# Kernel tuning notes

Hardware: AMD Instinct MI355X
Metric: run time of the kernel (lower is better)

## Reference

```python
import jax, jax.numpy as jnp
import numpy as np
import math


def _conv2d(x, w, b):
    # 3x3, stride 1, pad 1, NCHW / OIHW
    y = jax.lax.conv_general_dilated(x, w, (1, 1), ((1, 1), (1, 1)),
                                     dimension_numbers=('NCHW', 'OIHW', 'NCHW'))
    return y + b[None, :, None, None]


def _avgpool2(x):
    B, C, H, W = x.shape
    return x.reshape(B, C, H // 2, 2, W // 2, 2).mean(axis=(3, 5))


def setup_inputs() -> dict:
    key = jax.random.key(0)
    ks = jax.random.split(key, 12)
    B, H, W = 8, 512, 512
    x = jax.random.uniform(ks[0], (B, 3, H, W), dtype=jnp.float32)

    def conv_w(k, o, i):
        return jax.random.normal(k, (o, i, 3, 3), jnp.float32) / jnp.sqrt(jnp.float32(i * 9))

    def lin_w(k, o, i):
        return jax.random.normal(k, (o, i), jnp.float32) / jnp.sqrt(jnp.float32(i))

    return {
        'x': x,
        'w1': conv_w(ks[1], 16, 6),  'b1': jnp.zeros((16,), jnp.float32),
        'w2': conv_w(ks[2], 32, 16), 'b2': jnp.zeros((32,), jnp.float32),
        'w3': conv_w(ks[3], 64, 32), 'b3': jnp.zeros((64,), jnp.float32),
        'fw1': lin_w(ks[4], 256, 64),  'fb1': jnp.zeros((256,), jnp.float32),
        'fw2': lin_w(ks[5], 100, 256), 'fb2': jnp.zeros((100,), jnp.float32),
    }


def reference(x, w1, b1, w2, b2, w3, b3, fw1, fb1, fw2, fb2):
    B, C, H, W = x.shape
    # radial distance from image center (torch.meshgrid default = 'ij')
    a, b = jnp.meshgrid(jnp.arange(H), jnp.arange(W), indexing='ij')
    dist = jnp.sqrt((a - H / 2) ** 2 + (b - W / 2) ** 2).astype(jnp.float32)
    max_radius = math.sqrt(H * H + W * W) / 2

    xf = jnp.fft.fftn(x, axes=(-1, -2))
    # torch.fft.fftshift with no dim shifts ALL axes (incl. B, C); jnp matches.
    xf = jnp.fft.fftshift(xf)
    x_mag = jnp.log10(jnp.abs(xf) + 1)

    fi = jnp.concatenate([x, x_mag], axis=1)  # [B,6,H,W]
    y = jax.nn.relu(_conv2d(fi, w1, b1))
    y = _avgpool2(y)
    y = jax.nn.relu(_conv2d(y, w2, b2))
    y = _avgpool2(y)
    y = _conv2d(y, w3, b3)
    y = y.mean(axis=(2, 3))  # AdaptiveAvgPool2d((1,1)) -> [B,64]
    # note: NO activation between the two FC layers in the original
    value_set = jax.nn.leaky_relu((y @ fw1.T + fb1) @ fw2.T + fb2, 0.01)  # [B,100]

    # 100 radial ring bins; replace the 100-iter where-loop with bucketize+gather
    radius_set = max_radius * (jnp.arange(100, dtype=jnp.float32) + 1.0) * 0.01
    # bin i: radius_set[i-1] < dist <= radius_set[i]  ==  searchsorted left
    bin_idx = jnp.clip(jnp.searchsorted(radius_set, dist, side='left'), 0, 99)  # [H,W]
    fq_mask = value_set[:, bin_idx]  # [B,H,W] gather, same math as sum of ring masks

    low = xf * fq_mask[:, None, :, :]
    low = jnp.fft.ifftshift(low)
    low = jnp.fft.ifftn(low, axes=(-1, -2))
    lowpass = jnp.clip(low.real, 0.0, 1.0)
    return lowpass, fq_mask, value_set
```

## Files before the change

### kernel.cpp

```cpp
#include <hip/hip_runtime.h>
#include <math.h>

#define NPIX 262144
#define FSTR 513

__device__ __forceinline__ int brev9(int i) { return (int)(__brev((unsigned)i) >> 23); }

__device__ __forceinline__ void init_tw(float* twr, float* twi, int t) {
  if (t < 256) {
    float ang = -3.14159265358979323846f * (float)t / 256.0f;
    float s, c;
    sincosf(ang, &s, &c);
    twr[t] = c; twi[t] = s;
  }
}

template<bool FWD>
__device__ __forceinline__ void fft512x8(float* __restrict__ sr, float* __restrict__ si,
                                         const float* __restrict__ twr,
                                         const float* __restrict__ twi, int t) {
  const int c  = t >> 5;
  const int tq = t & 31;
  float* cr = sr + c * FSTR;
  float* ci = si + c * FSTR;
  #pragma unroll
  for (int sp = 0; sp < 4; sp++) {
    const int s = 2 * sp;
    const int h = 1 << s;
    __syncthreads();
    #pragma unroll
    for (int m = 0; m < 4; m++) {
      int q = tq + 32 * m;
      int j = q & (h - 1);
      int base = ((q >> s) << (s + 2)) | j;
      int i1 = j << (8 - s);
      int i2 = j << (7 - s);
      float w1r = twr[i1], w1i = FWD ? twi[i1] : -twi[i1];
      float w2r = twr[i2], w2i = FWD ? twi[i2] : -twi[i2];
      float ar = cr[base],         ai = ci[base];
      float br = cr[base + h],     bi = ci[base + h];
      float c2r = cr[base + 2*h],  c2i = ci[base + 2*h];
      float dr = cr[base + 3*h],   di = ci[base + 3*h];
      float wbr = br * w1r - bi * w1i, wbi = br * w1i + bi * w1r;
      float wdr = dr * w1r - di * w1i, wdi = dr * w1i + di * w1r;
      float t0r = ar + wbr,  t0i = ai + wbi;
      float t1r = ar - wbr,  t1i = ai - wbi;
      float t2r = c2r + wdr, t2i = c2i + wdi;
      float t3r = c2r - wdr, t3i = c2i - wdi;
      float u2r = t2r * w2r - t2i * w2i, u2i = t2r * w2i + t2i * w2r;
      float v3r = t3r * w2r - t3i * w2i, v3i = t3r * w2i + t3i * w2r;
      float u3r = FWD ? v3i : -v3i;
      float u3i = FWD ? -v3r : v3r;
      cr[base]         = t0r + u2r;  ci[base]         = t0i + u2i;
      cr[base + 2*h]   = t0r - u2r;  ci[base + 2*h]   = t0i - u2i;
      cr[base + h]     = t1r + u3r;  ci[base + h]     = t1i + u3i;
      cr[base + 3*h]   = t1r - u3r;  ci[base + 3*h]   = t1i - u3i;
    }
  }
  __syncthreads();
  #pragma unroll
  for (int m = 0; m < 8; m++) {
    int k = tq + 32 * m;
    float wr = twr[k], wi = FWD ? twi[k] : -twi[k];
    float vr = cr[k + 256], vi = ci[k + 256];
    float tr = vr * wr - vi * wi;
    float ti = vr * wi + vi * wr;
    float ur = cr[k], ui = ci[k];
    cr[k] = ur + tr;        ci[k] = ui + ti;
    cr[k + 256] = ur - tr;  ci[k + 256] = ui - ti;
  }
  __syncthreads();
}

__global__ __launch_bounds__(256) void k_fft_rows(const float* __restrict__ x,
                                                  float2* __restrict__ xf) {
  __shared__ float sr[8 * FSTR], si[8 * FSTR], twr[256], twi[256];
  int t = threadIdx.x;
  int img = blockIdx.x >> 6;
  int r0 = (blockIdx.x & 63) << 3;
  init_tw(twr, twi, t);
  const float4* p4 = (const float4*)(x + (size_t)img * NPIX + (size_t)r0 * 512);
  for (int e = t; e < 1024; e += 256) {
    int row = e >> 7, w = e & 127;
    float4 f = p4[e];
    float* cr = sr + row * FSTR;
    float* ci = si + row * FSTR;
    int p = 4 * w;
    cr[brev9(p)]     = f.x;  ci[brev9(p)]     = 0.0f;
    cr[brev9(p + 1)] = f.y;  ci[brev9(p + 1)] = 0.0f;
    cr[brev9(p + 2)] = f.z;  ci[brev9(p + 2)] = 0.0f;
    cr[brev9(p + 3)] = f.w;  ci[brev9(p + 3)] = 0.0f;
  }
  fft512x8<true>(sr, si, twr, twi, t);
  float4* q4 = (float4*)(xf + (size_t)img * NPIX + (size_t)r0 * 512);
  for (int e = t; e < 2048; e += 256) {
    int row = e >> 8, u = e & 255;
    const float* cr = sr + row * FSTR;
    const float* ci = si + row * FSTR;
    q4[e] = make_float4(cr[2 * u], ci[2 * u], cr[2 * u + 1], ci[2 * u + 1]);
  }
}

__global__ __launch_bounds__(256) void k_fft_cols(float2* __restrict__ xf,
                                                  float* __restrict__ xmag) {
  __shared__ float sr[8 * FSTR], si[8 * FSTR], twr[256], twi[256];
  int t = threadIdx.x;
  int img = blockIdx.x >> 6;
  int c0 = (blockIdx.x & 63) << 3;
  init_tw(twr, twi, t);
  float2* base = xf + (size_t)img * NPIX + c0;
  const int q = t & 3;
  const int j = (t >> 2) & 15;
  const int w = t >> 6;
  #pragma unroll
  for (int it = 0; it < 8; it++) {
    int row = 32 * j + 4 * it + w;
    float4 f = *(const float4*)(base + (size_t)row * 512 + 2 * q);
    int rr = brev9(row);
    sr[(2 * q) * FSTR + rr]     = f.x;  si[(2 * q) * FSTR + rr]     = f.y;
    sr[(2 * q + 1) * FSTR + rr] = f.z;  si[(2 * q + 1) * FSTR + rr] = f.w;
  }
  fft512x8<true>(sr, si, twr, twi, t);
  int sb = img / 3, sc = img - 3 * sb;
  int dimg = ((sb + 4) & 7) * 3 + (sc + 1) % 3;
  float* xb = xmag + (size_t)dimg * NPIX + (c0 ^ 256);
  const int rg = t >> 2;
  #pragma unroll
  for (int it = 0; it < 8; it++) {
    int row = 64 * it + rg;
    float a0 = sr[(2 * q) * FSTR + row],     b0 = si[(2 * q) * FSTR + row];
    float a1 = sr[(2 * q + 1) * FSTR + row], b1 = si[(2 * q + 1) * FSTR + row];
    *(float4*)(base + (size_t)row * 512 + 2 * q) = make_float4(a0, b0, a1, b1);
    float m0 = log10f(sqrtf(a0 * a0 + b0 * b0) + 1.0f);
    float m1 = log10f(sqrtf(a1 * a1 + b1 * b1) + 1.0f);
    *(float2*)(xb + (size_t)(row ^ 256) * 512 + 2 * q) = make_float2(m0, m1);
  }
}

__global__ __launch_bounds__(256) void k_conv1(const float* __restrict__ x,
                                               const float* __restrict__ xmag,
                                               const float* __restrict__ w1,
                                               const float* __restrict__ b1,
                                               float* __restrict__ out) {
  __shared__ float tile[2][18 * 132 + 8];
  const int t = threadIdx.x;
  const int tx = t & 31, ty = t >> 5;
  const int PC0 = blockIdx.x * 64;
  const int PR0 = blockIdx.y * 8;
  const int b  = blockIdx.z >> 1;
  const int og = (blockIdx.z & 1) * 8;
  const int R0 = PR0 * 2 - 1;
  const int C0 = PC0 * 2 - 1;

  int li[10], gi[10];
  bool okf[10];
  #pragma unroll
  for (int k = 0; k < 10; k++) {
    int e = t + 256 * k;
    bool valid = e < 2340;
    int i = e / 130, j = e - i * 130;
    int rr = R0 + i, cc = C0 + j;
    bool ok = valid && ((unsigned)rr < 512u) && ((unsigned)cc < 512u);
    li[k] = valid ? (i * 132 + j) : (18 * 132);
    gi[k] = ok ? (rr * 512 + cc) : 0;
    okf[k] = ok;
  }

  float acc[8][8];
  #pragma unroll
  for (int o = 0; o < 8; o++)
    #pragma unroll
    for (int q = 0; q < 8; q++) acc[o][q] = 0.0f;

  const float* xb = x + (size_t)(b * 3) * NPIX;
  const float* mb = xmag + (size_t)(b * 3) * NPIX;

  float ld[10];
  #pragma unroll
  for (int k = 0; k < 10; k++) ld[k] = okf[k] ? xb[gi[k]] : 0.0f;
  #pragma unroll
  for (int k = 0; k < 10; k++) tile[0][li[k]] = ld[k];
  __syncthreads();

  for (int ic = 0; ic < 6; ic++) {
    if (ic < 5) {
      const float* sn = (ic + 1 < 3) ? (xb + (size_t)(ic + 1) * NPIX)
                                     : (mb + (size_t)(ic - 2) * NPIX);
      #pragma unroll
      for (int k = 0; k < 10; k++) ld[k] = okf[k] ? sn[gi[k]] : 0.0f;
    }
    const float* cur = tile[ic & 1];
    float patch[4][6];
    #pragma unroll
    for (int dy = 0; dy < 4; dy++) {
      const float* rp = cur + (2 * ty + dy) * 132 + 4 * tx;
      float4 f = *(const float4*)rp;
      float2 g = *(const float2*)(rp + 4);
      patch[dy][0] = f.x; patch[dy][1] = f.y; patch[dy][2] = f.z;
      patch[dy][3] = f.w; patch[dy][4] = g.x; patch[dy][5] = g.y;
    }
    #pragma unroll
    for (int o = 0; o < 8; o++) {
      const float* wk = w1 + (size_t)((og + o) * 6 + ic) * 9;
      float k0 = wk[0], k1 = wk[1], k2 = wk[2], k3 = wk[3], k4 = wk[4],
            k5 = wk[5], k6 = wk[6], k7 = wk[7], k8 = wk[8];
      #pragma unroll
      for (int py = 0; py < 2; py++)
        #pragma unroll
        for (int px = 0; px < 4; px++) {
          acc[o][py * 4 + px] +=
              k0 * patch[py][px]     + k1 * patch[py][px + 1]     + k2 * patch[py][px + 2]
            + k3 * patch[py + 1][px] + k4 * patch[py + 1][px + 1] + k5 * patch[py + 1][px + 2]
            + k6 * patch[py + 2][px] + k7 * patch[py + 2][px + 1] + k8 * patch[py + 2][px + 2];
        }
    }
    if (ic < 5) {
      float* nxt = tile[(ic + 1) & 1];
      #pragma unroll
      for (int k = 0; k < 10; k++) nxt[li[k]] = ld[k];
      __syncthreads();
    }
  }
  #pragma unroll
  for (int o = 0; o < 8; o++) {
    float bias = b1[og + o];
    float p0 = fmaxf(acc[o][0] + bias, 0.0f) + fmaxf(acc[o][1] + bias, 0.0f)
             + fmaxf(acc[o][4] + bias, 0.0f) + fmaxf(acc[o][5] + bias, 0.0f);
    float p1 = fmaxf(acc[o][2] + bias, 0.0f) + fmaxf(acc[o][3] + bias, 0.0f)
             + fmaxf(acc[o][6] + bias, 0.0f) + fmaxf(acc[o][7] + bias, 0.0f);
    float2* q = (float2*)(out + ((size_t)(b * 16 + og + o) * 256 + PR0 + ty) * 256 + PC0 + 2 * tx);
    *q = make_float2(p0 * 0.25f, p1 * 0.25f);
  }
}

__global__ __launch_bounds__(256) void k_conv2(const float* __restrict__ in,
                                               const float* __restrict__ w2,
                                               const float* __restrict__ b2,
                                               float* __restrict__ S) {
  __shared__ float tile[2][18 * 68 + 8];
  __shared__ float wsum[4][8];
  const int t = threadIdx.x;
  const int tx = t & 31, ty = t >> 5;
  const int bx = blockIdx.x, by = blockIdx.y;
  const int PC0 = bx * 32;
  const int PR0 = by * 8;
  const int b  = blockIdx.z >> 2;
  const int og = (blockIdx.z & 3) * 8;
  const int R0 = PR0 * 2 - 1;
  const int C0 = PC0 * 2 - 1;

  int li[5], gi[5];
  bool okf[5];
  #pragma unroll
  for (int k = 0; k < 5; k++) {
    int e = t + 256 * k;
    bool valid = e < 1188;
    int i = e / 66, j = e - 66 * i;
    int rr = R0 + i, cc = C0 + j;
    bool ok = valid && ((unsigned)rr < 256u) && ((unsigned)cc < 256u);
    li[k] = valid ? (i * 68 + j) : (18 * 68);
    gi[k] = ok ? (rr * 256 + cc) : 0;
    okf[k] = ok;
  }

  float acc[8][4];
  #pragma unroll
  for (int o = 0; o < 8; o++)
    #pragma unroll
    for (int q = 0; q < 4; q++) acc[o][q] = 0.0f;

  const float* inb = in + (size_t)(b * 16) * 65536;

  float ld[5];
  #pragma unroll
  for (int k = 0; k < 5; k++) ld[k] = okf[k] ? inb[gi[k]] : 0.0f;
  #pragma unroll
  for (int k = 0; k < 5; k++) tile[0][li[k]] = ld[k];
  __syncthreads();

  for (int ic = 0; ic < 16; ic++) {
    if (ic < 15) {
      const float* sn = inb + (size_t)(ic + 1) * 65536;
      #pragma unroll
      for (int k = 0; k < 5; k++) ld[k] = okf[k] ? sn[gi[k]] : 0.0f;
    }
    const float* cur = tile[ic & 1];
    float patch[4][4];
    #pragma unroll
    for (int dy = 0; dy < 4; dy++) {
      const float* rp = cur + (2 * ty + dy) * 68 + 2 * tx;
      float2 f0 = *(const float2*)rp;
      float2 f1 = *(const float2*)(rp + 2);
      patch[dy][0] = f0.x; patch[dy][1] = f0.y;
      patch[dy][2] = f1.x; patch[dy][3] = f1.y;
    }
    #pragma unroll
    for (int o = 0; o < 8; o++) {
      const float* wk = w2 + (size_t)((og + o) * 16 + ic) * 9;
      float k0 = wk[0], k1 = wk[1], k2 = wk[2], k3 = wk[3], k4 = wk[4],
            k5 = wk[5], k6 = wk[6], k7 = wk[7], k8 = wk[8];
      #pragma unroll
      for (int py = 0; py < 2; py++)
        #pragma unroll
        for (int px = 0; px < 2; px++) {
          acc[o][py * 2 + px] +=
              k0 * patch[py][px]     + k1 * patch[py][px + 1]     + k2 * patch[py][px + 2]
            + k3 * patch[py + 1][px] + k4 * patch[py + 1][px + 1] + k5 * patch[py + 1][px + 2]
            + k6 * patch[py + 2][px] + k7 * patch[py + 2][px + 1] + k8 * patch[py + 2][px + 2];
        }
    }
    if (ic < 15) {
      float* nxt = tile[(ic + 1) & 1];
      #pragma unroll
      for (int k = 0; k < 5; k++) nxt[li[k]] = ld[k];
      __syncthreads();
    }
  }

  const int lane = t & 63;
  const int wid = t >> 6;
  float* Sb0 = S + (size_t)(b * 32 + og) * 9;
  #pragma unroll
  for (int o = 0; o < 8; o++) {
    float bias = b2[og + o];
    float v = (fmaxf(acc[o][0] + bias, 0.0f) + fmaxf(acc[o][1] + bias, 0.0f)
             + fmaxf(acc[o][2] + bias, 0.0f) + fmaxf(acc[o][3] + bias, 0.0f)) * 0.25f;
    float* Sb = Sb0 + o * 9;
    float ts = v;
    #pragma unroll
    for (int off = 32; off > 0; off >>= 1) ts += __shfl_down(ts, off);
    if (lane == 0) wsum[wid][o] = ts;
    if (by == 0) {
      float e = (ty == 0) ? v : 0.0f;
      #pragma unroll
      for (int off = 32; off > 0; off >>= 1) e += __shfl_down(e, off);
      if (lane == 0) atomicAdd(&Sb[1], e);
    }
    if (by == 15) {
      float e = (ty == 7) ? v : 0.0f;
      #pragma unroll
      for (int off = 32; off > 0; off >>= 1) e += __shfl_down(e, off);
      if (lane == 0) atomicAdd(&Sb[2], e);
    }
    if (bx == 0 && tx == 0)  atomicAdd(&Sb[3], v);
    if (bx == 3 && tx == 31) atomicAdd(&Sb[4], v);
    if (bx == 0 && by == 0  && t == 0)   Sb[5] = v;
    if (bx == 3 && by == 0  && t == 31)  Sb[6] = v;
    if (bx == 0 && by == 15 && t == 224) Sb[7] = v;
    if (bx == 3 && by == 15 && t == 255) Sb[8] = v;
  }
  __syncthreads();
  if (t < 8)
    atomicAdd(&Sb0[t * 9], wsum[0][t] + wsum[1][t] + wsum[2][t] + wsum[3][t]);
}

__global__ __launch_bounds__(256) void k_fc(const float* __restrict__ S,
                                            const float* __restrict__ w3,
                                            const float* __restrict__ b3,
                                            const float* __restrict__ fw1,
                                            const float* __restrict__ fb1,
                                            const float* __restrict__ fw2,
                                            const float* __restrict__ fb2,
                                            float* __restrict__ vs_out) {
  __shared__ float Sp[2304];
  __shared__ float y[512];
  __shared__ float h1[2048];
  int t = threadIdx.x;
  for (int e = t; e < 2304; e += 256) {
    int cell = e / 9, k = e - 9 * cell;
    int dy = k / 3, dx = k - 3 * dy;
    const float* s = S + cell * 9;
    float v = s[0];
    if (dy == 0) v -= s[2];
    if (dy == 2) v -= s[1];
    if (dx == 0) v -= s[4];
    if (dx == 2) v -= s[3];
    if (dy == 0 && dx == 0) v += s[8];
    if (dy == 0 && dx == 2) v += s[7];
    if (dy == 2 && dx == 0) v += s[6];
    if (dy == 2 && dx == 2) v += s[5];
    Sp[e] = v;
  }
  __syncthreads();
  for (int e = t; e < 512; e += 256) {
    int b = e >> 6, o = e & 63;
    const float* wrow = w3 + (size_t)o * 288;
    const float* sp = Sp + b * 288;
    float s = 0.0f;
    #pragma unroll 4
    for (int k = 0; k < 288; k++) s += wrow[k] * sp[k];
    y[e] = b3[o] + s * (1.0f / 16384.0f);
  }
  __syncthreads();
  for (int e = t; e < 2048; e += 256) {
    int b = e >> 8, j = e & 255;
    float s = fb1[j];
    for (int k = 0; k < 64; k++) s += y[b * 64 + k] * fw1[j * 64 + k];
    h1[e] = s;
  }
  __syncthreads();
  for (int e = t; e < 800; e += 256) {
    int b = e / 100, i = e - 100 * b;
    float s = fb2[i];
    for (int j = 0; j < 256; j++) s += h1[b * 256 + j] * fw2[i * 256 + j];
    vs_out[e] = (s >= 0.0f) ? s : 0.01f * s;
  }
}

__global__ __launch_bounds__(256) void k_mask(const float* __restrict__ vs,
                                              float* __restrict__ fq_mask) {
  int idx = blockIdx.x * 256 + threadIdx.x;
  int h = idx >> 9, w = idx & 511;
  float da = (float)h - 256.0f, db = (float)w - 256.0f;
  float dist = sqrtf(da * da + db * db);
  int lo = 0, hi = 100;
  while (lo < hi) {
    int mid = (lo + hi) >> 1;
    float r = (362.03867196751236f * (float)(mid + 1)) * 0.01f;
    if (r < dist) lo = mid + 1; else hi = mid;
  }
  int bin = lo > 99 ? 99 : lo;
  #pragma unroll
  for (int b = 0; b < 8; b++)
    fq_mask[(size_t)b * NPIX + idx] = vs[b * 100 + bin];
}

__global__ __launch_bounds__(256) void k_ifft_rows_mod(float2* __restrict__ xf,
                                                       const float* __restrict__ fq_mask) {
  __shared__ float sr[8 * FSTR], si[8 * FSTR], twr[256], twi[256];
  int t = threadIdx.x;
  int img = blockIdx.x >> 6;
  int r0 = (blockIdx.x & 63) << 3;
  int bm = ((img / 3) + 4) & 7;
  init_tw(twr, twi, t);
  const float* mbase = fq_mask + (size_t)bm * NPIX;
  float4* base4 = (float4*)(xf + (size_t)img * NPIX + (size_t)r0 * 512);
  for (int e = t; e < 2048; e += 256) {
    int u = (e & 3) | (((e >> 2) & 15) << 3) | (((e >> 6) & 1) << 2) | (((e >> 7) & 1) << 7);
    int row = e >> 8;
    float4 f = base4[row * 256 + u];
    int p0 = 2 * u;
    const float* mrow = mbase + (size_t)((r0 + row + 256) & 511) * 512;
    float2 m = *(const float2*)(mrow + ((p0 + 256) & 511));
    int rr0 = brev9(p0);
    float* cr = sr + row * FSTR;
    float* ci = si + row * FSTR;
    cr[rr0]       = f.x * m.x;  ci[rr0]       = f.y * m.x;
    cr[rr0 + 256] = f.z * m.y;  ci[rr0 + 256] = f.w * m.y;
  }
  fft512x8<false>(sr, si, twr, twi, t);
  for (int e = t; e < 2048; e += 256) {
    int row = e >> 8, u = e & 255;
    const float* cr = sr + row * FSTR;
    const float* ci = si + row * FSTR;
    base4[e] = make_float4(cr[2 * u], ci[2 * u], cr[2 * u + 1], ci[2 * u + 1]);
  }
}

__global__ __launch_bounds__(256) void k_ifft_cols_out(const float2* __restrict__ xf,
                                                       float* __restrict__ lowpass) {
  __shared__ float sr[8 * FSTR], si[8 * FSTR], twr[256], twi[256];
  int t = threadIdx.x;
  int img = blockIdx.x >> 6;
  int c0 = (blockIdx.x & 63) << 3;
  init_tw(twr, twi, t);
  const float2* base = xf + (size_t)img * NPIX + c0;
  const int q = t & 3;
  const int j = (t >> 2) & 15;
  const int w = t >> 6;
  #pragma unroll
  for (int it = 0; it < 8; it++) {
    int row = 32 * j + 4 * it + w;
    float4 f = *(const float4*)(base + (size_t)row * 512 + 2 * q);
    int rr = brev9(row);
    sr[(2 * q) * FSTR + rr]     = f.x;  si[(2 * q) * FSTR + rr]     = f.y;
    sr[(2 * q + 1) * FSTR + rr] = f.z;  si[(2 * q + 1) * FSTR + rr] = f.w;
  }
  fft512x8<false>(sr, si, twr, twi, t);
  const float sc = 1.0f / 262144.0f;
  float* obase = lowpass + (size_t)img * NPIX + c0;
  const int rg = t >> 2;
  #pragma unroll
  for (int it = 0; it < 8; it++) {
    int row = 64 * it + rg;
    float v0 = fminf(fmaxf(sr[(2 * q) * FSTR + row] * sc, 0.0f), 1.0f);
    float v1 = fminf(fmaxf(sr[(2 * q + 1) * FSTR + row] * sc, 0.0f), 1.0f);
    *(float2*)(obase + (size_t)row * 512 + 2 * q) = make_float2(v0, v1);
  }
}

extern "C" void kernel_launch(void* const* d_in, const int* in_sizes, int n_in,
                              void* d_out, int out_size, void* d_ws, size_t ws_size,
                              hipStream_t stream) {
  const float* x   = (const float*)d_in[0];
  const float* w1  = (const float*)d_in[1];
  const float* b1  = (const float*)d_in[2];
  const float* w2  = (const float*)d_in[3];
  const float* b2  = (const float*)d_in[4];
  const float* w3  = (const float*)d_in[5];
  const float* b3  = (const float*)d_in[6];
  const float* fw1 = (const float*)d_in[7];
  const float* fb1 = (const float*)d_in[8];
  const float* fw2 = (const float*)d_in[9];
  const float* fb2 = (const float*)d_in[10];

  float* lowpass = (float*)d_out;
  float* fq_mask = lowpass + 6291456;
  float* vs      = fq_mask + 2097152;

  float* base    = (float*)d_ws;
  float2* xf     = (float2*)base;
  float* xmag    = base + 12582912;
  float* pooled1 = xmag + 6291456;
  float* S       = pooled1 + 8388608;

  k_fft_rows<<<dim3(24 * 64), 256, 0, stream>>>(x, xf);
  k_fft_cols<<<dim3(24 * 64), 256, 0, stream>>>(xf, xmag);

  k_conv1<<<dim3(4, 32, 16), 256, 0, stream>>>(x, xmag, w1, b1, pooled1);
  hipMemsetAsync(S, 0, 2304 * sizeof(float), stream);
  k_conv2<<<dim3(4, 16, 32), 256, 0, stream>>>(pooled1, w2, b2, S);

  k_fc<<<1, 256, 0, stream>>>(S, w3, b3, fw1, fb1, fw2, fb2, vs);
  k_mask<<<1024, 256, 0, stream>>>(vs, fq_mask);

  k_ifft_rows_mod<<<dim3(24 * 64), 256, 0, stream>>>(xf, fq_mask);
  k_ifft_cols_out<<<dim3(24 * 64), 256, 0, stream>>>(xf, lowpass);
}
```

Before: 392.8 us.

## Deepen conv2 input prefetch to triple-buffered LDS with two-ahead register loads

The conv2 kernel moves from a double-buffered shared tile with one-channel-ahead global prefetch to a triple-buffered tile with loads issued two channels ahead. The aim is to hide more global-memory latency behind the per-channel FMA work. In exchange it uses more LDS and extra registers for a second load buffer, which may lower occupancy. The ld[(r+1)&1] indexing inside the loop may force the register array into scratch unless the loop is unrolled.

Result: no change. 397.8 us (+1.3%).

```diff
diff --git a/kernel.cpp b/kernel.cpp
--- a/kernel.cpp
+++ b/kernel.cpp
@@ -237,7 +237,7 @@
                                                const float* __restrict__ w2,
                                                const float* __restrict__ b2,
                                                float* __restrict__ S) {
-  __shared__ float tile[2][18 * 68 + 8];
+  __shared__ float tile[3][18 * 68 + 8];
   __shared__ float wsum[4][8];
   const int t = threadIdx.x;
   const int tx = t & 31, ty = t >> 5;
@@ -271,20 +271,32 @@
 
   const float* inb = in + (size_t)(b * 16) * 65536;
 
-  float ld[5];
-  #pragma unroll
-  for (int k = 0; k < 5; k++) ld[k] = okf[k] ? inb[gi[k]] : 0.0f;
-  #pragma unroll
-  for (int k = 0; k < 5; k++) tile[0][li[k]] = ld[k];
-  __syncthreads();
-
-  for (int ic = 0; ic < 16; ic++) {
-    if (ic < 15) {
-      const float* sn = inb + (size_t)(ic + 1) * 65536;
-      #pragma unroll
-      for (int k = 0; k < 5; k++) ld[k] = okf[k] ? sn[gi[k]] : 0.0f;
-    }
-    const float* cur = tile[ic & 1];
+  float ld[2][5];
+  #pragma unroll
+  for (int k = 0; k < 5; k++) ld[0][k] = okf[k] ? inb[gi[k]] : 0.0f;
+  #pragma unroll
+  for (int k = 0; k < 5; k++) tile[0][li[k]] = ld[0][k];
+  {
+    const float* s1 = inb + 65536;
+    #pragma unroll
+    for (int k = 0; k < 5; k++) ld[0][k] = okf[k] ? s1[gi[k]] : 0.0f;
+    #pragma unroll
+    for (int k = 0; k < 5; k++) tile[1][li[k]] = ld[0][k];
+  }
+  __syncthreads();
+  {
+    const float* s2 = inb + 2 * 65536;
+    #pragma unroll
+    for (int k = 0; k < 5; k++) ld[0][k] = okf[k] ? s2[gi[k]] : 0.0f;
+  }
+
+  for (int r = 0; r < 16; r++) {
+    if (r + 3 < 16) {
+      const float* sn = inb + (size_t)(r + 3) * 65536;
+      #pragma unroll
+      for (int k = 0; k < 5; k++) ld[(r + 1) & 1][k] = okf[k] ? sn[gi[k]] : 0.0f;
+    }
+    const float* cur = tile[r % 3];
     float patch[4][4];
     #pragma unroll
     for (int dy = 0; dy < 4; dy++) {
@@ -296,7 +308,7 @@
     }
     #pragma unroll
     for (int o = 0; o < 8; o++) {
-      const float* wk = w2 + (size_t)((og + o) * 16 + ic) * 9;
+      const float* wk = w2 + (size_t)((og + o) * 16 + r) * 9;
       float k0 = wk[0], k1 = wk[1], k2 = wk[2], k3 = wk[3], k4 = wk[4],
             k5 = wk[5], k6 = wk[6], k7 = wk[7], k8 = wk[8];
       #pragma unroll
@@ -309,10 +321,10 @@
             + k6 * patch[py + 2][px] + k7 * patch[py + 2][px + 1] + k8 * patch[py + 2][px + 2];
         }
     }
-    if (ic < 15) {
-      float* nxt = tile[(ic + 1) & 1];
-      #pragma unroll
-      for (int k = 0; k < 5; k++) nxt[li[k]] = ld[k];
+    if (r + 2 < 16) {
+      float* nxt = tile[(r + 2) % 3];
+      #pragma unroll
+      for (int k = 0; k < 5; k++) nxt[li[k]] = ld[r & 1][k];
       __syncthreads();
     }
   }
```
